# Performance work log

Measured on AMD Instinct MI355X. Metric: run time of the kernel, lower is better.

Reference implementation:

```python
import jax, jax.numpy as jnp
import numpy as np

P = 2        # patch size (all 3 dims)
NB = 8       # num_bands
N = 16       # d_state
DTR = 8      # dt_rank = d_model // 16
DCONV = 4    # d_conv
SMAX = 2.0   # smax_dt = smax_B = smax_C


def _ln(x, g, b):
    mu = x.mean(-1, keepdims=True)
    v = ((x - mu) ** 2).mean(-1, keepdims=True)
    return (x - mu) / jnp.sqrt(v + 1e-5) * g + b


def _silu(x):
    return x * jax.nn.sigmoid(x)


def _ssm_layer(x, band, m, rho, Win, bin_, convw, convb, Wx, Wdt, bdt, Alog, Dp,
               Wout, bout, edt, eB, eC, wr, wm):
    # x: [B, L, d_model] -> bidirectional conditioned selective scan (BiFCSSM)
    Bsz, L, _ = x.shape
    ED = convw.shape[0]
    xz = x @ Win + bin_
    xp, z = xz[..., :ED], xz[..., ED:]
    # depthwise causal conv1d over L
    xpad = jnp.pad(xp, ((0, 0), (DCONV - 1, 0), (0, 0)))
    xc = sum(xpad[:, k:k + L, :] * convw[:, k] for k in range(DCONV)) + convb
    xc = _silu(xc)
    dbl = xc @ Wx                                    # [B,L,DTR+2N]
    dt = jax.nn.softplus(dbl[..., :DTR] @ Wdt + bdt)  # [B,L,ED]
    # band/radius/mask conditioned modulation of delta, B, C
    s_dt = SMAX * jax.nn.sigmoid(edt[band][None] + wr[0] * rho[None] + wm[0] * m)
    s_B = SMAX * jax.nn.sigmoid(eB[band][None] + wr[1] * rho[None] + wm[1] * m)
    s_C = SMAX * jax.nn.sigmoid(eC[band][None] + wr[2] * rho[None] + wm[2] * m)
    dt = dt * s_dt[..., None]
    Bm = dbl[..., DTR:DTR + N] * s_B[..., None]       # [B,L,N]
    Cm = dbl[..., DTR + N:] * s_C[..., None]          # [B,L,N]
    A = -jnp.exp(Alog)                                # [ED,N]
    dA = jnp.exp(dt[..., None] * A)                   # [B,L,ED,N]
    dBu = (dA - 1.0) / A * Bm[:, :, None, :] * xc[..., None]   # exact ZOH
    dA_s = jnp.moveaxis(dA, 1, 0)
    dBu_s = jnp.moveaxis(dBu, 1, 0)
    C_s = jnp.moveaxis(Cm, 1, 0)
    h0 = jnp.zeros((Bsz, ED, N), x.dtype)

    def step(h, inp):
        a, bu, c = inp
        h = a * h + bu
        return h, jnp.einsum('ben,bn->be', h, c)

    _, yf = jax.lax.scan(step, h0, (dA_s, dBu_s, C_s))
    _, yb = jax.lax.scan(step, h0, (dA_s, dBu_s, C_s), reverse=True)
    y = jnp.moveaxis(yf + yb, 0, 1) + Dp * xc
    y = y * _silu(z)
    return y @ Wout + bout


def _fwd(kspace_ri, mask, pe_w, pe_b, pu_w, pu_b, ln_g, ln_b, fn_g, fn_b,
         cond_band, cond_rad_w, cond_mask_w, l0_Win, l0_bin, l0_convw, l0_convb,
         l0_Wx, l0_Wdt, l0_bdt, l0_Alog, l0_D, l0_Wout, l0_bout, l0_edt, l0_eB,
         l0_eC, l0_wr, l0_wm):
    Bsz, C, nx, ny, nz = kspace_ri.shape
    gx, gy, gz = nx // P, ny // P, nz // P
    L = gx * gy * gz
    # patch embed (Conv3d, kernel==stride) as blocked einsum
    xr = kspace_ri.reshape(Bsz, C, gx, P, gy, P, gz, P)
    x = jnp.einsum('bcxiyjzk,dcijk->bdxyz', xr, pe_w) + pe_b[None, :, None, None, None]
    DM = x.shape[1]
    x = x.reshape(Bsz, DM, L).transpose(0, 2, 1)               # [B,L,D]
    m = mask.reshape(Bsz, 1, gx, P, gy, P, gz, P).mean(axis=(3, 5, 7)).reshape(Bsz, L)
    m = jnp.clip(m, 0.0, 1.0)
    # raster scan ordering: identity permutation, rho_bar, band ids
    rho = jnp.arange(L, dtype=x.dtype) / float(L - 1)
    band = jnp.clip(jnp.floor(rho * NB).astype(jnp.int32), 0, NB - 1)
    # condition tokens
    cond = cond_band[band][None] + rho[None, :, None] * cond_rad_w + m[:, :, None] * cond_mask_w
    h = _ln(x + cond, ln_g, ln_b)
    h = h + _ssm_layer(_ln(h, fn_g, fn_b), band, m, rho, l0_Win, l0_bin, l0_convw,
                       l0_convb, l0_Wx, l0_Wdt, l0_bdt, l0_Alog, l0_D, l0_Wout,
                       l0_bout, l0_edt, l0_eB, l0_eC, l0_wr, l0_wm)
    # patch unembed (ConvTranspose3d, kernel==stride) as blocked einsum
    hg = h.transpose(0, 2, 1).reshape(Bsz, DM, gx, gy, gz)
    out = jnp.einsum('bdxyz,dcijk->bcxiyjzk', hg, pu_w).reshape(Bsz, C, nx, ny, nz)
    out = out + pu_b[None, :, None, None, None]
    return kspace_ri + out


def setup_inputs() -> dict:
    key = jax.random.key(0)
    ks = jax.random.split(key, 24)
    ED, DM, CIN = 256, 128, 16

    def nrm(k, shape, s):
        return jax.random.normal(k, shape, jnp.float32) * s

    return {
        'kspace_ri': jax.random.normal(ks[0], (1, CIN, 64, 64, 16), jnp.float32),
        'mask': jax.random.uniform(ks[1], (1, 1, 64, 64, 16), jnp.float32),
        'pe_w': nrm(ks[2], (DM, CIN, P, P, P), 0.09),
        'pe_b': nrm(ks[3], (DM,), 0.02),
        'pu_w': nrm(ks[4], (DM, CIN, P, P, P), 0.05),
        'pu_b': jnp.zeros((CIN,), jnp.float32),
        'ln_g': jnp.ones((DM,), jnp.float32),
        'ln_b': jnp.zeros((DM,), jnp.float32),
        'fn_g': jnp.ones((DM,), jnp.float32),
        'fn_b': jnp.zeros((DM,), jnp.float32),
        'cond_band': nrm(ks[5], (NB, DM), 0.02),
        'cond_rad_w': nrm(ks[6], (DM,), 0.02),
        'cond_mask_w': nrm(ks[7], (DM,), 0.02),
        'l0_Win': nrm(ks[8], (DM, 2 * ED), 0.05),
        'l0_bin': jnp.zeros((2 * ED,), jnp.float32),
        'l0_convw': nrm(ks[9], (ED, DCONV), 0.2),
        'l0_convb': jnp.zeros((ED,), jnp.float32),
        'l0_Wx': nrm(ks[10], (ED, DTR + 2 * N), 0.05),
        'l0_Wdt': nrm(ks[11], (DTR, ED), 0.1),
        'l0_bdt': jnp.full((ED,), -3.0, jnp.float32),
        'l0_Alog': jnp.log(jnp.tile(jnp.arange(1, N + 1, dtype=jnp.float32), (ED, 1))),
        'l0_D': jnp.ones((ED,), jnp.float32),
        'l0_Wout': nrm(ks[12], (ED, DM), 0.05),
        'l0_bout': jnp.zeros((DM,), jnp.float32),
        'l0_edt': nrm(ks[13], (NB,), 0.1),
        'l0_eB': nrm(ks[14], (NB,), 0.1),
        'l0_eC': nrm(ks[15], (NB,), 0.1),
        'l0_wr': nrm(ks[16], (3,), 0.1),
        'l0_wm': nrm(ks[17], (3,), 0.1),
    }


def reference(kspace_ri, mask, pe_w, pe_b, pu_w, pu_b, ln_g, ln_b, fn_g, fn_b,
              cond_band, cond_rad_w, cond_mask_w, l0_Win, l0_bin, l0_convw,
              l0_convb, l0_Wx, l0_Wdt, l0_bdt, l0_Alog, l0_D, l0_Wout, l0_bout,
              l0_edt, l0_eB, l0_eC, l0_wr, l0_wm):
    return _fwd(kspace_ri, mask, pe_w, pe_b, pu_w, pu_b, ln_g, ln_b, fn_g, fn_b,
                cond_band, cond_rad_w, cond_mask_w, l0_Win, l0_bin, l0_convw,
                l0_convb, l0_Wx, l0_Wdt, l0_bdt, l0_Alog, l0_D, l0_Wout, l0_bout,
                l0_edt, l0_eB, l0_eC, l0_wr, l0_wm)
```

## Files before the change

### kernel.cpp

```cpp
#include <hip/hip_runtime.h>
#include <hip/hip_bf16.h>

#define L_TOK 8192
#define NCh 256
#define CLh 32
#define LOG2E 1.44269504088896f

typedef short bf16x8 __attribute__((ext_vector_type(8)));
typedef float f32x4 __attribute__((ext_vector_type(4)));

static __device__ __forceinline__ float nexp2(float x) {
#if __has_builtin(__builtin_amdgcn_exp2f)
    return __builtin_amdgcn_exp2f(x);
#else
    return exp2f(x);
#endif
}
static __device__ __forceinline__ float sigm(float x) {
    return 1.f / (1.f + nexp2(-x * LOG2E));
}

static __device__ __forceinline__ ushort f2bf(float x) {
    union { float f; uint u; } v; v.f = x;
    uint r = v.u + 0x7fffu + ((v.u >> 16) & 1u);
// ... 62 lines not shown
        }
    }
    ushort h, lo; f2hl(v, &h, &lo);
    wH[i] = h; wL[i] = lo;
}

__global__ __launch_bounds__(256) void embed_ln_k(const float* __restrict__ ks,
                                                  const ushort* __restrict__ wH, const ushort* __restrict__ wL,
                                                  const float* __restrict__ pe_b, const float* __restrict__ cond_band,
                                                  const float* __restrict__ cond_rad, const float* __restrict__ cond_mask,
                                                  const float* __restrict__ mbuf,
                                                  const float* __restrict__ ln_g, const float* __restrict__ ln_b,
                                                  const float* __restrict__ fn_g, const float* __restrict__ fn_b,
                                                  float* __restrict__ h_,
                                                  ushort* __restrict__ hnH, ushort* __restrict__ hnL) {
    __shared__ __align__(16) char smem[46080];
    ushort (*AsH)[72] = (ushort(*)[72])(smem);
    ushort (*AsL)[72] = (ushort(*)[72])(smem + 4608);
    ushort (*BsH)[72] = (ushort(*)[72])(smem + 9216);
    ushort (*BsL)[72] = (ushort(*)[72])(smem + 27648);
    float  (*Cs)[132] = (float(*)[132])(smem);

    const int tid = threadIdx.x;
    const int lane = tid & 63, wn = tid >> 6;
    const int ln = lane & 15, q = lane >> 4;
    const int mb = blockIdx.x * 32;

    f32x4 acc[2][2];
#pragma unroll
    for (int rb = 0; rb < 2; ++rb)
#pragma unroll
        for (int cb = 0; cb < 2; ++cb) acc[rb][cb] = (f32x4){0.f, 0.f, 0.f, 0.f};

    for (int kc = 0; kc < 128; kc += 64) {
        __syncthreads();
        for (int u = tid; u < 2048; u += 256) {
            int r = u >> 6, kk = u & 63;
            int l = mb + r, k = kc + kk;
            int cc = k >> 3, ijk = k & 7;
            int xg = l >> 8, yg = (l >> 3) & 31, zg = l & 7;
            int i2 = (ijk >> 2) & 1, j2 = (ijk >> 1) & 1, k2 = ijk & 1;
            float v = ks[cc * 65536 + (2 * xg + i2) * 1024 + (2 * yg + j2) * 16 + 2 * zg + k2];
            ushort h, lo; f2hl(v, &h, &lo);
            AsH[r][kk] = h; AsL[r][kk] = lo;
        }
        for (int u = tid; u < 1024; u += 256) {
            int n = u >> 3, g = u & 7;
            *(uint4*)&BsH[n][g * 8] = *(const uint4*)&wH[W_PE + n * 128 + kc + g * 8];
            *(uint4*)&BsL[n][g * 8] = *(const uint4*)&wL[W_PE + n * 128 + kc + g * 8];
        }
        __syncthreads();
#pragma unroll
        for (int ks_ = 0; ks_ < 64; ks_ += 32) {
            const int kk = ks_ + q * 8;
            bf16x8 ah[2], al[2], bh[2], bl[2];
#pragma unroll
            for (int rb = 0; rb < 2; ++rb) {
                ah[rb] = *(const bf16x8*)&AsH[rb * 16 + ln][kk];
                al[rb] = *(const bf16x8*)&AsL[rb * 16 + ln][kk];
            }
#pragma unroll
            for (int cb = 0; cb < 2; ++cb) {
                bh[cb] = *(const bf16x8*)&BsH[wn * 32 + cb * 16 + ln][kk];
                bl[cb] = *(const bf16x8*)&BsL[wn * 32 + cb * 16 + ln][kk];
            }
#pragma unroll
            for (int rb = 0; rb < 2; ++rb)
#pragma unroll
                for (int cb = 0; cb < 2; ++cb) {
                    acc[rb][cb] = __builtin_amdgcn_mfma_f32_16x16x32_bf16(ah[rb], bh[cb], acc[rb][cb], 0, 0, 0);
                    acc[rb][cb] = __builtin_amdgcn_mfma_f32_16x16x32_bf16(ah[rb], bl[cb], acc[rb][cb], 0, 0, 0);
                    acc[rb][cb] = __builtin_amdgcn_mfma_f32_16x16x32_bf16(al[rb], bh[cb], acc[rb][cb], 0, 0, 0);
                }
        }
    }
    __syncthreads();
#pragma unroll
    for (int rb = 0; rb < 2; ++rb) {
#pragma unroll
        for (int cb = 0; cb < 2; ++cb) {
#pragma unroll
            for (int r = 0; r < 4; ++r) {
                int row = rb * 16 + q * 4 + r;
                int col = wn * 32 + cb * 16 + ln;
                int l = mb + row;
                float rho = (float)l * (1.0f / 8191.0f);
                int band = min(7, (int)(rho * 8.0f));
                Cs[row][col] = acc[rb][cb][r] + pe_b[col] + cond_band[band * 128 + col]
                               + rho * cond_rad[col] + mbuf[l] * cond_mask[col];
            }
        }
    }
    __syncthreads();
    {
        int row = tid >> 3, j = tid & 7;
        int l = mb + row;
        float v16[16];
        float s = 0.f, s2 = 0.f;
#pragma unroll
        for (int i = 0; i < 16; ++i) {
            float v = Cs[row][j * 16 + i];
            v16[i] = v; s += v; s2 += v * v;
        }
#pragma unroll
        for (int o = 1; o < 8; o <<= 1) { s += __shfl_xor(s, o, 8); s2 += __shfl_xor(s2, o, 8); }
        float mu = s * (1.f / 128.f);
        float var = s2 * (1.f / 128.f) - mu * mu;
        float rstd = rsqrtf(fmaxf(var, 0.f) + 1e-5f);
        float hv[16];
        s = 0.f; s2 = 0.f;
#pragma unroll
        for (int i = 0; i < 16; ++i) {
            int col = j * 16 + i;
            float h = (v16[i] - mu) * rstd * ln_g[col] + ln_b[col];
            hv[i] = h; s += h; s2 += h * h;
        }
#pragma unroll
        for (int i = 0; i < 16; i += 4)
            *(float4*)&h_[(size_t)l * 128 + j * 16 + i] = make_float4(hv[i], hv[i + 1], hv[i + 2], hv[i + 3]);
#pragma unroll
        for (int o = 1; o < 8; o <<= 1) { s += __shfl_xor(s, o, 8); s2 += __shfl_xor(s2, o, 8); }
        mu = s * (1.f / 128.f);
        var = s2 * (1.f / 128.f) - mu * mu;
        rstd = rsqrtf(fmaxf(var, 0.f) + 1e-5f);
        union { ushort u[16]; uint4 v4[2]; } oh, ol;
#pragma unroll
        for (int i = 0; i < 16; ++i) {
            int col = j * 16 + i;
            float o2 = (hv[i] - mu) * rstd * fn_g[col] + fn_b[col];
            ushort hh, ll; f2hl(o2, &hh, &ll);
            oh.u[i] = hh; ol.u[i] = ll;
        }
        *(uint4*)&hnH[(size_t)l * 128 + j * 16] = oh.v4[0];
        *(uint4*)&hnH[(size_t)l * 128 + j * 16 + 8] = oh.v4[1];
        *(uint4*)&hnL[(size_t)l * 128 + j * 16] = ol.v4[0];
        *(uint4*)&hnL[(size_t)l * 128 + j * 16 + 8] = ol.v4[1];
    }
}

__global__ __launch_bounds__(256) void win_k(const ushort* __restrict__ Ah, const ushort* __restrict__ Al,
                                             const ushort* __restrict__ wH, const ushort* __restrict__ wL,
                                             const float* __restrict__ bin_,
                                             float* __restrict__ xp, float* __restrict__ sz) {
    __shared__ ushort AsH[128][72], AsL[128][72];
    __shared__ ushort BsH[64][72], BsL[64][72];
    const int tid = threadIdx.x;
    const int lane = tid & 63, wave = tid >> 6;
    const int wm = wave & 1, wn = wave >> 1;
    const int ln = lane & 15, q = lane >> 4;
    const int mb = blockIdx.x * 128, nb = blockIdx.y * 64;

    f32x4 acc[4][2];
#pragma unroll
    for (int rb = 0; rb < 4; ++rb)
#pragma unroll
        for (int cb = 0; cb < 2; ++cb) acc[rb][cb] = (f32x4){0.f, 0.f, 0.f, 0.f};

    for (int kc = 0; kc < 128; kc += 64) {
        __syncthreads();
        for (int u = tid; u < 1024; u += 256) {
            int r = u >> 3, g = u & 7;
            size_t go = (size_t)(mb + r) * 128 + kc + g * 8;
            *(uint4*)&AsH[r][g * 8] = *(const uint4*)&Ah[go];
            *(uint4*)&AsL[r][g * 8] = *(const uint4*)&Al[go];
        }
        for (int u = tid; u < 512; u += 256) {
            int n = u >> 3, g = u & 7;
            size_t go = (size_t)(W_WIN) + (size_t)(nb + n) * 128 + kc + g * 8;
            *(uint4*)&BsH[n][g * 8] = *(const uint4*)&wH[go];
            *(uint4*)&BsL[n][g * 8] = *(const uint4*)&wL[go];
        }
        __syncthreads();
#pragma unroll
        for (int ks_ = 0; ks_ < 64; ks_ += 32) {
            const int kk = ks_ + q * 8;
            bf16x8 ah[4], al[4], bh[2], bl[2];
#pragma unroll
            for (int rb = 0; rb < 4; ++rb) {
                ah[rb] = *(const bf16x8*)&AsH[wm * 64 + rb * 16 + ln][kk];
                al[rb] = *(const bf16x8*)&AsL[wm * 64 + rb * 16 + ln][kk];
            }
#pragma unroll
            for (int cb = 0; cb < 2; ++cb) {
                bh[cb] = *(const bf16x8*)&BsH[wn * 32 + cb * 16 + ln][kk];
                bl[cb] = *(const bf16x8*)&BsL[wn * 32 + cb * 16 + ln][kk];
            }
#pragma unroll
            for (int rb = 0; rb < 4; ++rb)
#pragma unroll
                for (int cb = 0; cb < 2; ++cb) {
                    acc[rb][cb] = __builtin_amdgcn_mfma_f32_16x16x32_bf16(ah[rb], bh[cb], acc[rb][cb], 0, 0, 0);
                    acc[rb][cb] = __builtin_amdgcn_mfma_f32_16x16x32_bf16(ah[rb], bl[cb], acc[rb][cb], 0, 0, 0);
                    acc[rb][cb] = __builtin_amdgcn_mfma_f32_16x16x32_bf16(al[rb], bh[cb], acc[rb][cb], 0, 0, 0);
                }
        }
    }
#pragma unroll
    for (int rb = 0; rb < 4; ++rb)
#pragma unroll
        for (int cb = 0; cb < 2; ++cb)
#pragma unroll
            for (int r = 0; r < 4; ++r) {
                int l = mb + wm * 64 + rb * 16 + q * 4 + r;
                int col = nb + wn * 32 + cb * 16 + ln;
                float v = acc[rb][cb][r] + bin_[col];
                if (col < 256) {
                    xp[(size_t)l * 256 + col] = v;
                } else {
                    sz[(size_t)l * 256 + (col - 256)] = v * sigm(v);
                }
            }
}

__global__ __launch_bounds__(256) void conv_k(const float* __restrict__ xp, const float* __restrict__ convw,
                                              const float* __restrict__ convb, float* __restrict__ xc) {
    int id = blockIdx.x * 256 + threadIdx.x;
    int l = id >> 6, e4 = (id & 63) * 4;
    float4 cw[4];
// ... 15 lines not shown
    float4 r;
    r.x = o[0] * sigm(o[0]);
    r.y = o[1] * sigm(o[1]);
    r.z = o[2] * sigm(o[2]);
    r.w = o[3] * sigm(o[3]);
    *(float4*)&xc[(size_t)l * 256 + e4] = r;
}

__global__ __launch_bounds__(256) void proj_k(const float* __restrict__ xc,
                                              const ushort* __restrict__ wH, const ushort* __restrict__ wL,
                                              const float* __restrict__ bdt, const float* __restrict__ mbuf,
                                              const float* __restrict__ edt, const float* __restrict__ eB,
                                              const float* __restrict__ eC, const float* __restrict__ wr,
                                              const float* __restrict__ wm,
                                              float* __restrict__ dt, float* __restrict__ Bm, float* __restrict__ Cm) {
    __shared__ ushort AsH[128][72], AsL[128][72];
    __shared__ ushort BsH[64][72], BsL[64][72];
    const int tid = threadIdx.x;
    const int lane = tid & 63, wave = tid >> 6;
    const int wm_ = wave & 1, wn = wave >> 1;
    const int ln = lane & 15, q = lane >> 4;
    const int mb = blockIdx.x * 128, nb = blockIdx.y * 64;

    f32x4 acc[4][2];
#pragma unroll
    for (int rb = 0; rb < 4; ++rb)
#pragma unroll
        for (int cb = 0; cb < 2; ++cb) acc[rb][cb] = (f32x4){0.f, 0.f, 0.f, 0.f};

    for (int kc = 0; kc < 256; kc += 64) {
        __syncthreads();
        for (int u = tid; u < 2048; u += 256) {
            int r = u >> 4, kq = u & 15;
            float4 v = *(const float4*)&xc[(size_t)(mb + r) * 256 + kc + kq * 4];
            union { ushort u[4]; uint2 v2; } hh, ll;
            f2hl(v.x, &hh.u[0], &ll.u[0]); f2hl(v.y, &hh.u[1], &ll.u[1]);
            f2hl(v.z, &hh.u[2], &ll.u[2]); f2hl(v.w, &hh.u[3], &ll.u[3]);
            *(uint2*)&AsH[r][kq * 4] = hh.v2;
            *(uint2*)&AsL[r][kq * 4] = ll.v2;
        }
        for (int u = tid; u < 512; u += 256) {
            int n = u >> 3, g = u & 7;
            size_t go = (size_t)(W_PROJ) + (size_t)(nb + n) * 256 + kc + g * 8;
            *(uint4*)&BsH[n][g * 8] = *(const uint4*)&wH[go];
            *(uint4*)&BsL[n][g * 8] = *(const uint4*)&wL[go];
        }
        __syncthreads();
#pragma unroll
        for (int ks_ = 0; ks_ < 64; ks_ += 32) {
            const int kk = ks_ + q * 8;
            bf16x8 ah[4], al[4], bh[2], bl[2];
#pragma unroll
            for (int rb = 0; rb < 4; ++rb) {
                ah[rb] = *(const bf16x8*)&AsH[wm_ * 64 + rb * 16 + ln][kk];
                al[rb] = *(const bf16x8*)&AsL[wm_ * 64 + rb * 16 + ln][kk];
            }
#pragma unroll
            for (int cb = 0; cb < 2; ++cb) {
                bh[cb] = *(const bf16x8*)&BsH[wn * 32 + cb * 16 + ln][kk];
                bl[cb] = *(const bf16x8*)&BsL[wn * 32 + cb * 16 + ln][kk];
            }
#pragma unroll
            for (int rb = 0; rb < 4; ++rb)
#pragma unroll
                for (int cb = 0; cb < 2; ++cb) {
                    acc[rb][cb] = __builtin_amdgcn_mfma_f32_16x16x32_bf16(ah[rb], bh[cb], acc[rb][cb], 0, 0, 0);
                    acc[rb][cb] = __builtin_amdgcn_mfma_f32_16x16x32_bf16(ah[rb], bl[cb], acc[rb][cb], 0, 0, 0);
                    acc[rb][cb] = __builtin_amdgcn_mfma_f32_16x16x32_bf16(al[rb], bh[cb], acc[rb][cb], 0, 0, 0);
                }
        }
    }
#pragma unroll
    for (int rb = 0; rb < 4; ++rb)
#pragma unroll
        for (int cb = 0; cb < 2; ++cb)
#pragma unroll
            for (int r = 0; r < 4; ++r) {
                int l = mb + wm_ * 64 + rb * 16 + q * 4 + r;
                int col = nb + wn * 32 + cb * 16 + ln;
                float v = acc[rb][cb][r];
                float rho = (float)l * (1.0f / 8191.0f);
                int band = min(7, (int)(rho * 8.0f));
                float mv = mbuf[l];
                if (col < 256) {
                    float sc0 = 2.0f * sigm(edt[band] + wr[0] * rho + wm[0] * mv);
                    float v2 = v + bdt[col];
                    float sp = (v2 > 20.f) ? v2 : log1pf(expf(v2));
                    dt[(size_t)l * 256 + col] = sp * sc0;
                } else if (col < 272) {
                    float sc1 = 2.0f * sigm(eB[band] + wr[1] * rho + wm[1] * mv);
                    Bm[(size_t)l * 16 + (col - 256)] = v * sc1;
                } else if (col < 288) {
                    float sc2 = 2.0f * sigm(eC[band] + wr[2] * rho + wm[2] * mv);
// ... 80 lines not shown
            if (PHASE == 1) yp[(size_t)(base + p) * 256 + e] = y;
        }
#pragma unroll
        for (int j = 0; j < 8; ++j) { cu[j] = nu[j]; cx[j] = nx[j]; }
    }
    if (PHASE == 0) {
#pragma unroll
        for (int j = 0; j < 4; ++j) {
            float4 hv = make_float4(h[4 * j], h[4 * j + 1], h[4 * j + 2], h[4 * j + 3]);
            *(float4*)&Hb[hofs + 4 * j] = hv;
        }
        if (dir == 0) sdtb[c * 256 + e] = sdt;
    }
}

__global__ __launch_bounds__(256) void combine_k(float* __restrict__ Hb, const float* __restrict__ sdtb,
                                                 const float* __restrict__ Alog) {
    int id = blockIdx.x * 256 + threadIdx.x;
    int dir = id >> 12, en = id & 4095, e = en >> 4;
    float A2 = -nexp2(Alog[en] * LOG2E) * LOG2E;
    float hi = 0.f;
    for (int g = 0; g < NCh / 8; ++g) {
        float Pv[8], qv[8];
#pragma unroll
        for (int j = 0; j < 8; ++j) {
            int c = dir ? (NCh - 1 - (g * 8 + j)) : (g * 8 + j);
            Pv[j] = sdtb[c * 256 + e];
            qv[j] = Hb[(size_t)(dir * NCh + c) * 4096 + en];
        }
#pragma unroll
        for (int j = 0; j < 8; ++j) {
            int c = dir ? (NCh - 1 - (g * 8 + j)) : (g * 8 + j);
            float P = nexp2(A2 * Pv[j]);
            Hb[(size_t)(dir * NCh + c) * 4096 + en] = hi;
            hi = P * hi + qv[j];
        }
    }
}

__global__ __launch_bounds__(256) void wout_k(const float* __restrict__ yf, const float* __restrict__ yb,
                                              const float* __restrict__ xc, const float* __restrict__ sz,
                                              const float* __restrict__ Dp,
                                              const ushort* __restrict__ wH, const ushort* __restrict__ wL,
                                              const float* __restrict__ bout, const float* __restrict__ h_,
                                              ushort* __restrict__ hfH, ushort* __restrict__ hfL) {
    __shared__ ushort AsH[64][72], AsL[64][72];
    __shared__ ushort BsH[64][72], BsL[64][72];
    const int tid = threadIdx.x;
    const int lane = tid & 63, wave = tid >> 6;
    const int wm = wave & 1, wn = wave >> 1;
    const int ln = lane & 15, q = lane >> 4;
    const int mb = blockIdx.x * 64, nb = blockIdx.y * 64;

    f32x4 acc[2][2];
#pragma unroll
    for (int rb = 0; rb < 2; ++rb)
#pragma unroll
        for (int cb = 0; cb < 2; ++cb) acc[rb][cb] = (f32x4){0.f, 0.f, 0.f, 0.f};

    for (int kc = 0; kc < 256; kc += 64) {
        __syncthreads();
        for (int u = tid; u < 1024; u += 256) {
            int r = u >> 4, kq = u & 15;
            size_t go = (size_t)(mb + r) * 256 + kc + kq * 4;
            float4 a = *(const float4*)&yf[go];
            float4 b = *(const float4*)&yb[go];
            float4 x = *(const float4*)&xc[go];
            float4 s = *(const float4*)&sz[go];
            float4 d = *(const float4*)&Dp[kc + kq * 4];
            float v0 = (a.x + b.x + d.x * x.x) * s.x;
            float v1 = (a.y + b.y + d.y * x.y) * s.y;
            float v2 = (a.z + b.z + d.z * x.z) * s.z;
            float v3 = (a.w + b.w + d.w * x.w) * s.w;
            union { ushort u[4]; uint2 v2; } hh, ll;
            f2hl(v0, &hh.u[0], &ll.u[0]); f2hl(v1, &hh.u[1], &ll.u[1]);
            f2hl(v2, &hh.u[2], &ll.u[2]); f2hl(v3, &hh.u[3], &ll.u[3]);
            *(uint2*)&AsH[r][kq * 4] = hh.v2;
            *(uint2*)&AsL[r][kq * 4] = ll.v2;
        }
        for (int u = tid; u < 512; u += 256) {
            int n = u >> 3, g = u & 7;
            size_t go = (size_t)(W_WOUT) + (size_t)(nb + n) * 256 + kc + g * 8;
            *(uint4*)&BsH[n][g * 8] = *(const uint4*)&wH[go];
            *(uint4*)&BsL[n][g * 8] = *(const uint4*)&wL[go];
        }
        __syncthreads();
#pragma unroll
        for (int ks_ = 0; ks_ < 64; ks_ += 32) {
            const int kk = ks_ + q * 8;
            bf16x8 ah[2], al[2], bh[2], bl[2];
#pragma unroll
            for (int rb = 0; rb < 2; ++rb) {
                ah[rb] = *(const bf16x8*)&AsH[wm * 32 + rb * 16 + ln][kk];
                al[rb] = *(const bf16x8*)&AsL[wm * 32 + rb * 16 + ln][kk];
            }
#pragma unroll
            for (int cb = 0; cb < 2; ++cb) {
                bh[cb] = *(const bf16x8*)&BsH[wn * 32 + cb * 16 + ln][kk];
                bl[cb] = *(const bf16x8*)&BsL[wn * 32 + cb * 16 + ln][kk];
            }
#pragma unroll
            for (int rb = 0; rb < 2; ++rb)
#pragma unroll
                for (int cb = 0; cb < 2; ++cb) {
                    acc[rb][cb] = __builtin_amdgcn_mfma_f32_16x16x32_bf16(ah[rb], bh[cb], acc[rb][cb], 0, 0, 0);
                    acc[rb][cb] = __builtin_amdgcn_mfma_f32_16x16x32_bf16(ah[rb], bl[cb], acc[rb][cb], 0, 0, 0);
                    acc[rb][cb] = __builtin_amdgcn_mfma_f32_16x16x32_bf16(al[rb], bh[cb], acc[rb][cb], 0, 0, 0);
                }
        }
    }
#pragma unroll
    for (int rb = 0; rb < 2; ++rb)
#pragma unroll
        for (int cb = 0; cb < 2; ++cb)
#pragma unroll
            for (int r = 0; r < 4; ++r) {
                int l = mb + wm * 32 + rb * 16 + q * 4 + r;
                int col = nb + wn * 32 + cb * 16 + ln;
                float v = acc[rb][cb][r] + bout[col] + h_[(size_t)l * 128 + col];
                ushort hh, ll; f2hl(v, &hh, &ll);
                hfH[(size_t)l * 128 + col] = hh;
                hfL[(size_t)l * 128 + col] = ll;
            }
}

__global__ __launch_bounds__(256) void unembed_k(const ushort* __restrict__ Ah, const ushort* __restrict__ Al,
                                                 const ushort* __restrict__ wH, const ushort* __restrict__ wL,
                                                 const float* __restrict__ pu_b, const float* __restrict__ ks,
                                                 float* __restrict__ out) {
    __shared__ ushort AsH[64][72], AsL[64][72];
    __shared__ ushort BsH[64][72], BsL[64][72];
    const int tid = threadIdx.x;
    const int lane = tid & 63, wave = tid >> 6;
    const int wm = wave & 1, wn = wave >> 1;
    const int ln = lane & 15, q = lane >> 4;
    const int mb = blockIdx.x * 64, nb = blockIdx.y * 64;

    f32x4 acc[2][2];
#pragma unroll
    for (int rb = 0; rb < 2; ++rb)
#pragma unroll
        for (int cb = 0; cb < 2; ++cb) acc[rb][cb] = (f32x4){0.f, 0.f, 0.f, 0.f};

    for (int kc = 0; kc < 128; kc += 64) {
        __syncthreads();
        for (int u = tid; u < 512; u += 256) {
            int r = u >> 3, g = u & 7;
            size_t go = (size_t)(mb + r) * 128 + kc + g * 8;
            *(uint4*)&AsH[r][g * 8] = *(const uint4*)&Ah[go];
            *(uint4*)&AsL[r][g * 8] = *(const uint4*)&Al[go];
        }
        for (int u = tid; u < 512; u += 256) {
            int n = u >> 3, g = u & 7;
            size_t go = (size_t)(W_PU) + (size_t)(nb + n) * 128 + kc + g * 8;
            *(uint4*)&BsH[n][g * 8] = *(const uint4*)&wH[go];
            *(uint4*)&BsL[n][g * 8] = *(const uint4*)&wL[go];
        }
        __syncthreads();
#pragma unroll
        for (int ks_ = 0; ks_ < 64; ks_ += 32) {
            const int kk = ks_ + q * 8;
            bf16x8 ah[2], al[2], bh[2], bl[2];
#pragma unroll
            for (int rb = 0; rb < 2; ++rb) {
                ah[rb] = *(const bf16x8*)&AsH[wm * 32 + rb * 16 + ln][kk];
                al[rb] = *(const bf16x8*)&AsL[wm * 32 + rb * 16 + ln][kk];
            }
#pragma unroll
            for (int cb = 0; cb < 2; ++cb) {
                bh[cb] = *(const bf16x8*)&BsH[wn * 32 + cb * 16 + ln][kk];
                bl[cb] = *(const bf16x8*)&BsL[wn * 32 + cb * 16 + ln][kk];
            }
#pragma unroll
            for (int rb = 0; rb < 2; ++rb)
#pragma unroll
                for (int cb = 0; cb < 2; ++cb) {
                    acc[rb][cb] = __builtin_amdgcn_mfma_f32_16x16x32_bf16(ah[rb], bh[cb], acc[rb][cb], 0, 0, 0);
                    acc[rb][cb] = __builtin_amdgcn_mfma_f32_16x16x32_bf16(ah[rb], bl[cb], acc[rb][cb], 0, 0, 0);
                    acc[rb][cb] = __builtin_amdgcn_mfma_f32_16x16x32_bf16(al[rb], bh[cb], acc[rb][cb], 0, 0, 0);
                }
        }
    }
#pragma unroll
    for (int rb = 0; rb < 2; ++rb)
#pragma unroll
        for (int cb = 0; cb < 2; ++cb)
#pragma unroll
            for (int r = 0; r < 4; ++r) {
                int l = mb + wm * 32 + rb * 16 + q * 4 + r;
                int col = nb + wn * 32 + cb * 16 + ln;
                int xg = l >> 8, yg = (l >> 3) & 31, zg = l & 7;
                int c = col >> 3, ijk = col & 7;
                int i2 = (ijk >> 2) & 1, j2 = (ijk >> 1) & 1, k2 = ijk & 1;
                size_t idx = (size_t)((c * 64 + 2 * xg + i2) * 64 + (2 * yg + j2)) * 16 + 2 * zg + k2;
                out[idx] = acc[rb][cb][r] + pu_b[c] + ks[idx];
            }
}

extern "C" void kernel_launch(void* const* d_in, const int* in_sizes, int n_in,
                              void* d_out, int out_size, void* d_ws, size_t ws_size,
                              hipStream_t stream) {
    const float* ks    = (const float*)d_in[0];
    const float* mask  = (const float*)d_in[1];
    const float* pe_w  = (const float*)d_in[2];
    const float* pe_b  = (const float*)d_in[3];
    const float* pu_w  = (const float*)d_in[4];
    const float* pu_b  = (const float*)d_in[5];
    const float* ln_g  = (const float*)d_in[6];
    const float* ln_b  = (const float*)d_in[7];
    const float* fn_g  = (const float*)d_in[8];
    const float* fn_b  = (const float*)d_in[9];
// ... 22 lines not shown
    size_t o = 0;
    auto alloc = [&](size_t bytes) { char* p = base + o; o += (bytes + 255) & ~(size_t)255; return p; };
    float*  mbuf = (float*)alloc(32768);
    ushort* wH   = (ushort*)alloc(W_TOT * 2);
    ushort* wL   = (ushort*)alloc(W_TOT * 2);
    float*  h_   = (float*)alloc(4194304);
    ushort* hnH  = (ushort*)alloc(2097152);
    ushort* hnL  = (ushort*)alloc(2097152);
    float*  xp   = (float*)alloc(8388608);
    float*  sz   = (float*)alloc(8388608);
    float*  xc   = (float*)alloc(8388608);
    float*  dt   = (float*)alloc(8388608);
    float*  Bm   = (float*)alloc(524288);
    float*  Cm   = (float*)alloc(524288);
    float*  Hb   = (float*)alloc(8388608);
    float*  sdtb = (float*)alloc(262144);
    float*  yf   = (float*)alloc(8388608);
    float*  yb   = (float*)alloc(8388608);
    ushort* hfH  = (ushort*)alloc(2097152);
    ushort* hfL  = (ushort*)alloc(2097152);

    prep_k<<<864, 256, 0, stream>>>(pe_w, Win, Wx, Wdt, Wout, pu_w, mask, wH, wL, mbuf);
    embed_ln_k<<<256, 256, 0, stream>>>(ks, wH, wL, pe_b, cond_band, cond_rad, cond_mask, mbuf,
                                        ln_g, ln_b, fn_g, fn_b, h_, hnH, hnL);
    win_k<<<dim3(64, 8), 256, 0, stream>>>(hnH, hnL, wH, wL, bin_, xp, sz);
    conv_k<<<2048, 256, 0, stream>>>(xp, convw, convb, xc);
    proj_k<<<dim3(64, 5), 256, 0, stream>>>(xc, wH, wL, bdt, mbuf, edt, eB, eC, wr, wm, dt, Bm, Cm);
    scan_k<0><<<dim3(NCh, 2), 256, 0, stream>>>(dt, xc, Bm, Cm, Alog, Hb, sdtb, nullptr, nullptr);
    combine_k<<<32, 256, 0, stream>>>(Hb, sdtb, Alog);
    scan_k<1><<<dim3(NCh, 2), 256, 0, stream>>>(dt, xc, Bm, Cm, Alog, Hb, sdtb, yf, yb);
    wout_k<<<dim3(128, 2), 256, 0, stream>>>(yf, yb, xc, sz, Dp, wH, wL, bout, h_, hfH, hfL);
    unembed_k<<<dim3(128, 2), 256, 0, stream>>>(hfH, hfL, wH, wL, pu_b, ks, out);
}
```

Before: 258.8 us.

## Halve GEMM row tiles to double grid sizes and split combine output buffer

Halves the M-tile size in the embed, Win, proj, Wout and unembed GEMM kernels, doubling their block counts so more CUs are busy on this small token count. The combine kernel now uses 64-thread blocks across 128 blocks and writes prefix states to a separate Hpre buffer instead of overwriting Hb in place. This trades weight-tile reuse per block for more parallelism, and adds an extra 8 MB workspace buffer.

```diff
diff --git a/kernel.cpp b/kernel.cpp
--- a/kernel.cpp
+++ b/kernel.cpp
@@ -100,27 +100,25 @@
                                                   const float* __restrict__ fn_g, const float* __restrict__ fn_b,
                                                   float* __restrict__ h_,
                                                   ushort* __restrict__ hnH, ushort* __restrict__ hnL) {
-    __shared__ __align__(16) char smem[46080];
+    __shared__ __align__(16) char smem[41472];
     ushort (*AsH)[72] = (ushort(*)[72])(smem);
-    ushort (*AsL)[72] = (ushort(*)[72])(smem + 4608);
-    ushort (*BsH)[72] = (ushort(*)[72])(smem + 9216);
-    ushort (*BsL)[72] = (ushort(*)[72])(smem + 27648);
+    ushort (*AsL)[72] = (ushort(*)[72])(smem + 2304);
+    ushort (*BsH)[72] = (ushort(*)[72])(smem + 4608);
+    ushort (*BsL)[72] = (ushort(*)[72])(smem + 23040);
     float  (*Cs)[132] = (float(*)[132])(smem);
 
     const int tid = threadIdx.x;
     const int lane = tid & 63, wn = tid >> 6;
     const int ln = lane & 15, q = lane >> 4;
-    const int mb = blockIdx.x * 32;
-
-    f32x4 acc[2][2];
-#pragma unroll
-    for (int rb = 0; rb < 2; ++rb)
-#pragma unroll
-        for (int cb = 0; cb < 2; ++cb) acc[rb][cb] = (f32x4){0.f, 0.f, 0.f, 0.f};
+    const int mb = blockIdx.x * 16;
+
+    f32x4 acc[2];
+    acc[0] = (f32x4){0.f, 0.f, 0.f, 0.f};
+    acc[1] = (f32x4){0.f, 0.f, 0.f, 0.f};
 
     for (int kc = 0; kc < 128; kc += 64) {
         __syncthreads();
-        for (int u = tid; u < 2048; u += 256) {
+        for (int u = tid; u < 1024; u += 256) {
             int r = u >> 6, kk = u & 63;
             int l = mb + r, k = kc + kk;
             int cc = k >> 3, ijk = k & 7;
@@ -139,11 +137,118 @@
 #pragma unroll
         for (int ks_ = 0; ks_ < 64; ks_ += 32) {
             const int kk = ks_ + q * 8;
+            bf16x8 ah = *(const bf16x8*)&AsH[ln][kk];
+            bf16x8 al = *(const bf16x8*)&AsL[ln][kk];
+#pragma unroll
+            for (int cb = 0; cb < 2; ++cb) {
+                bf16x8 bh = *(const bf16x8*)&BsH[wn * 32 + cb * 16 + ln][kk];
+                bf16x8 bl = *(const bf16x8*)&BsL[wn * 32 + cb * 16 + ln][kk];
+                acc[cb] = __builtin_amdgcn_mfma_f32_16x16x32_bf16(ah, bh, acc[cb], 0, 0, 0);
+                acc[cb] = __builtin_amdgcn_mfma_f32_16x16x32_bf16(ah, bl, acc[cb], 0, 0, 0);
+                acc[cb] = __builtin_amdgcn_mfma_f32_16x16x32_bf16(al, bh, acc[cb], 0, 0, 0);
+            }
+        }
+    }
+    __syncthreads();
+#pragma unroll
+    for (int cb = 0; cb < 2; ++cb) {
+#pragma unroll
+        for (int r = 0; r < 4; ++r) {
+            int row = q * 4 + r;
+            int col = wn * 32 + cb * 16 + ln;
+            int l = mb + row;
+            float rho = (float)l * (1.0f / 8191.0f);
+            int band = min(7, (int)(rho * 8.0f));
+            Cs[row][col] = acc[cb][r] + pe_b[col] + cond_band[band * 128 + col]
+                           + rho * cond_rad[col] + mbuf[l] * cond_mask[col];
+        }
+    }
+    __syncthreads();
+    {
+        int row = tid >> 4, j = tid & 15;
+        int l = mb + row;
+        float v8[8];
+        float s = 0.f, s2 = 0.f;
+#pragma unroll
+        for (int i = 0; i < 8; ++i) {
+            float v = Cs[row][j * 8 + i];
+            v8[i] = v; s += v; s2 += v * v;
+        }
+#pragma unroll
+        for (int o = 1; o < 16; o <<= 1) { s += __shfl_xor(s, o, 16); s2 += __shfl_xor(s2, o, 16); }
+        float mu = s * (1.f / 128.f);
+        float var = s2 * (1.f / 128.f) - mu * mu;
+        float rstd = rsqrtf(fmaxf(var, 0.f) + 1e-5f);
+        float hv[8];
+        s = 0.f; s2 = 0.f;
+#pragma unroll
+        for (int i = 0; i < 8; ++i) {
+            int col = j * 8 + i;
+            float h = (v8[i] - mu) * rstd * ln_g[col] + ln_b[col];
+            hv[i] = h; s += h; s2 += h * h;
+        }
+#pragma unroll
+        for (int i = 0; i < 8; i += 4)
+            *(float4*)&h_[(size_t)l * 128 + j * 8 + i] = make_float4(hv[i], hv[i + 1], hv[i + 2], hv[i + 3]);
+#pragma unroll
+        for (int o = 1; o < 16; o <<= 1) { s += __shfl_xor(s, o, 16); s2 += __shfl_xor(s2, o, 16); }
+        mu = s * (1.f / 128.f);
+        var = s2 * (1.f / 128.f) - mu * mu;
+        rstd = rsqrtf(fmaxf(var, 0.f) + 1e-5f);
+        union { ushort u[8]; uint4 v4; } oh, ol;
+#pragma unroll
+        for (int i = 0; i < 8; ++i) {
+            int col = j * 8 + i;
+            float o2 = (hv[i] - mu) * rstd * fn_g[col] + fn_b[col];
+            ushort hh, ll; f2hl(o2, &hh, &ll);
+            oh.u[i] = hh; ol.u[i] = ll;
+        }
+        *(uint4*)&hnH[(size_t)l * 128 + j * 8] = oh.v4;
+        *(uint4*)&hnL[(size_t)l * 128 + j * 8] = ol.v4;
+    }
+}
+
+__global__ __launch_bounds__(256) void win_k(const ushort* __restrict__ Ah, const ushort* __restrict__ Al,
+                                             const ushort* __restrict__ wH, const ushort* __restrict__ wL,
+                                             const float* __restrict__ bin_,
+                                             float* __restrict__ xp, float* __restrict__ sz) {
+    __shared__ ushort AsH[64][72], AsL[64][72];
+    __shared__ ushort BsH[64][72], BsL[64][72];
+    const int tid = threadIdx.x;
+    const int lane = tid & 63, wave = tid >> 6;
+    const int wm = wave & 1, wn = wave >> 1;
+    const int ln = lane & 15, q = lane >> 4;
+    const int mb = blockIdx.x * 64, nb = blockIdx.y * 64;
+
+    f32x4 acc[2][2];
+#pragma unroll
+    for (int rb = 0; rb < 2; ++rb)
+#pragma unroll
+        for (int cb = 0; cb < 2; ++cb) acc[rb][cb] = (f32x4){0.f, 0.f, 0.f, 0.f};
+
+    for (int kc = 0; kc < 128; kc += 64) {
+        __syncthreads();
+        for (int u = tid; u < 512; u += 256) {
+            int r = u >> 3, g = u & 7;
+            size_t go = (size_t)(mb + r) * 128 + kc + g * 8;
+            *(uint4*)&AsH[r][g * 8] = *(const uint4*)&Ah[go];
+            *(uint4*)&AsL[r][g * 8] = *(const uint4*)&Al[go];
+        }
+        for (int u = tid; u < 512; u += 256) {
+            int n = u >> 3, g = u & 7;
+            size_t go = (size_t)(W_WIN) + (size_t)(nb + n) * 128 + kc + g * 8;
+            *(uint4*)&BsH[n][g * 8] = *(const uint4*)&wH[go];
+            *(uint4*)&BsL[n][g * 8] = *(const uint4*)&wL[go];
+        }
+        __syncthreads();
+#pragma unroll
+        for (int ks_ = 0; ks_ < 64; ks_ += 32) {
+            const int kk = ks_ + q * 8;
             bf16x8 ah[2], al[2], bh[2], bl[2];
 #pragma unroll
             for (int rb = 0; rb < 2; ++rb) {
-                ah[rb] = *(const bf16x8*)&AsH[rb * 16 + ln][kk];
-                al[rb] = *(const bf16x8*)&AsL[rb * 16 + ln][kk];
+                ah[rb] = *(const bf16x8*)&AsH[wm * 32 + rb * 16 + ln][kk];
+                al[rb] = *(const bf16x8*)&AsL[wm * 32 + rb * 16 + ln][kk];
             }
 #pragma unroll
             for (int cb = 0; cb < 2; ++cb) {
@@ -160,134 +265,13 @@
                 }
         }
     }
-    __syncthreads();
-#pragma unroll
-    for (int rb = 0; rb < 2; ++rb) {
-#pragma unroll
-        for (int cb = 0; cb < 2; ++cb) {
+#pragma unroll
+    for (int rb = 0; rb < 2; ++rb)
+#pragma unroll
+        for (int cb = 0; cb < 2; ++cb)
 #pragma unroll
             for (int r = 0; r < 4; ++r) {
-                int row = rb * 16 + q * 4 + r;
-                int col = wn * 32 + cb * 16 + ln;
-                int l = mb + row;
-                float rho = (float)l * (1.0f / 8191.0f);
-                int band = min(7, (int)(rho * 8.0f));
-                Cs[row][col] = acc[rb][cb][r] + pe_b[col] + cond_band[band * 128 + col]
-                               + rho * cond_rad[col] + mbuf[l] * cond_mask[col];
-            }
-        }
-    }
-    __syncthreads();
-    {
-        int row = tid >> 3, j = tid & 7;
-        int l = mb + row;
-        float v16[16];
-        float s = 0.f, s2 = 0.f;
-#pragma unroll
-        for (int i = 0; i < 16; ++i) {
-            float v = Cs[row][j * 16 + i];
-            v16[i] = v; s += v; s2 += v * v;
-        }
-#pragma unroll
-        for (int o = 1; o < 8; o <<= 1) { s += __shfl_xor(s, o, 8); s2 += __shfl_xor(s2, o, 8); }
-        float mu = s * (1.f / 128.f);
-        float var = s2 * (1.f / 128.f) - mu * mu;
-        float rstd = rsqrtf(fmaxf(var, 0.f) + 1e-5f);
-        float hv[16];
-        s = 0.f; s2 = 0.f;
-#pragma unroll
-        for (int i = 0; i < 16; ++i) {
-            int col = j * 16 + i;
-            float h = (v16[i] - mu) * rstd * ln_g[col] + ln_b[col];
-            hv[i] = h; s += h; s2 += h * h;
-        }
-#pragma unroll
-        for (int i = 0; i < 16; i += 4)
-            *(float4*)&h_[(size_t)l * 128 + j * 16 + i] = make_float4(hv[i], hv[i + 1], hv[i + 2], hv[i + 3]);
-#pragma unroll
-        for (int o = 1; o < 8; o <<= 1) { s += __shfl_xor(s, o, 8); s2 += __shfl_xor(s2, o, 8); }
-        mu = s * (1.f / 128.f);
-        var = s2 * (1.f / 128.f) - mu * mu;
-        rstd = rsqrtf(fmaxf(var, 0.f) + 1e-5f);
-        union { ushort u[16]; uint4 v4[2]; } oh, ol;
-#pragma unroll
-        for (int i = 0; i < 16; ++i) {
-            int col = j * 16 + i;
-            float o2 = (hv[i] - mu) * rstd * fn_g[col] + fn_b[col];
-            ushort hh, ll; f2hl(o2, &hh, &ll);
-            oh.u[i] = hh; ol.u[i] = ll;
-        }
-        *(uint4*)&hnH[(size_t)l * 128 + j * 16] = oh.v4[0];
-        *(uint4*)&hnH[(size_t)l * 128 + j * 16 + 8] = oh.v4[1];
-        *(uint4*)&hnL[(size_t)l * 128 + j * 16] = ol.v4[0];
-        *(uint4*)&hnL[(size_t)l * 128 + j * 16 + 8] = ol.v4[1];
-    }
-}
-
-__global__ __launch_bounds__(256) void win_k(const ushort* __restrict__ Ah, const ushort* __restrict__ Al,
-                                             const ushort* __restrict__ wH, const ushort* __restrict__ wL,
-                                             const float* __restrict__ bin_,
-                                             float* __restrict__ xp, float* __restrict__ sz) {
-    __shared__ ushort AsH[128][72], AsL[128][72];
-    __shared__ ushort BsH[64][72], BsL[64][72];
-    const int tid = threadIdx.x;
-    const int lane = tid & 63, wave = tid >> 6;
-    const int wm = wave & 1, wn = wave >> 1;
-    const int ln = lane & 15, q = lane >> 4;
-    const int mb = blockIdx.x * 128, nb = blockIdx.y * 64;
-
-    f32x4 acc[4][2];
-#pragma unroll
-    for (int rb = 0; rb < 4; ++rb)
-#pragma unroll
-        for (int cb = 0; cb < 2; ++cb) acc[rb][cb] = (f32x4){0.f, 0.f, 0.f, 0.f};
-
-    for (int kc = 0; kc < 128; kc += 64) {
-        __syncthreads();
-        for (int u = tid; u < 1024; u += 256) {
-            int r = u >> 3, g = u & 7;
-            size_t go = (size_t)(mb + r) * 128 + kc + g * 8;
-            *(uint4*)&AsH[r][g * 8] = *(const uint4*)&Ah[go];
-            *(uint4*)&AsL[r][g * 8] = *(const uint4*)&Al[go];
-        }
-        for (int u = tid; u < 512; u += 256) {
-            int n = u >> 3, g = u & 7;
-            size_t go = (size_t)(W_WIN) + (size_t)(nb + n) * 128 + kc + g * 8;
-            *(uint4*)&BsH[n][g * 8] = *(const uint4*)&wH[go];
-            *(uint4*)&BsL[n][g * 8] = *(const uint4*)&wL[go];
-        }
-        __syncthreads();
-#pragma unroll
-        for (int ks_ = 0; ks_ < 64; ks_ += 32) {
-            const int kk = ks_ + q * 8;
-            bf16x8 ah[4], al[4], bh[2], bl[2];
-#pragma unroll
-            for (int rb = 0; rb < 4; ++rb) {
-                ah[rb] = *(const bf16x8*)&AsH[wm * 64 + rb * 16 + ln][kk];
-                al[rb] = *(const bf16x8*)&AsL[wm * 64 + rb * 16 + ln][kk];
-            }
-#pragma unroll
-            for (int cb = 0; cb < 2; ++cb) {
-                bh[cb] = *(const bf16x8*)&BsH[wn * 32 + cb * 16 + ln][kk];
-                bl[cb] = *(const bf16x8*)&BsL[wn * 32 + cb * 16 + ln][kk];
-            }
-#pragma unroll
-            for (int rb = 0; rb < 4; ++rb)
-#pragma unroll
-                for (int cb = 0; cb < 2; ++cb) {
-                    acc[rb][cb] = __builtin_amdgcn_mfma_f32_16x16x32_bf16(ah[rb], bh[cb], acc[rb][cb], 0, 0, 0);
-                    acc[rb][cb] = __builtin_amdgcn_mfma_f32_16x16x32_bf16(ah[rb], bl[cb], acc[rb][cb], 0, 0, 0);
-                    acc[rb][cb] = __builtin_amdgcn_mfma_f32_16x16x32_bf16(al[rb], bh[cb], acc[rb][cb], 0, 0, 0);
-                }
-        }
-    }
-#pragma unroll
-    for (int rb = 0; rb < 4; ++rb)
-#pragma unroll
-        for (int cb = 0; cb < 2; ++cb)
-#pragma unroll
-            for (int r = 0; r < 4; ++r) {
-                int l = mb + wm * 64 + rb * 16 + q * 4 + r;
+                int l = mb + wm * 32 + rb * 16 + q * 4 + r;
                 int col = nb + wn * 32 + cb * 16 + ln;
                 float v = acc[rb][cb][r] + bin_[col];
                 if (col < 256) {
@@ -333,23 +317,23 @@
                                               const float* __restrict__ eC, const float* __restrict__ wr,
                                               const float* __restrict__ wm,
                                               float* __restrict__ dt, float* __restrict__ Bm, float* __restrict__ Cm) {
-    __shared__ ushort AsH[128][72], AsL[128][72];
+    __shared__ ushort AsH[64][72], AsL[64][72];
     __shared__ ushort BsH[64][72], BsL[64][72];
     const int tid = threadIdx.x;
     const int lane = tid & 63, wave = tid >> 6;
     const int wm_ = wave & 1, wn = wave >> 1;
     const int ln = lane & 15, q = lane >> 4;
-    const int mb = blockIdx.x * 128, nb = blockIdx.y * 64;
-
-    f32x4 acc[4][2];
-#pragma unroll
-    for (int rb = 0; rb < 4; ++rb)
+    const int mb = blockIdx.x * 64, nb = blockIdx.y * 64;
+
+    f32x4 acc[2][2];
+#pragma unroll
+    for (int rb = 0; rb < 2; ++rb)
 #pragma unroll
         for (int cb = 0; cb < 2; ++cb) acc[rb][cb] = (f32x4){0.f, 0.f, 0.f, 0.f};
 
     for (int kc = 0; kc < 256; kc += 64) {
         __syncthreads();
-        for (int u = tid; u < 2048; u += 256) {
+        for (int u = tid; u < 1024; u += 256) {
             int r = u >> 4, kq = u & 15;
             float4 v = *(const float4*)&xc[(size_t)(mb + r) * 256 + kc + kq * 4];
             union { ushort u[4]; uint2 v2; } hh, ll;
@@ -368,11 +352,11 @@
 #pragma unroll
         for (int ks_ = 0; ks_ < 64; ks_ += 32) {
             const int kk = ks_ + q * 8;
-            bf16x8 ah[4], al[4], bh[2], bl[2];
-#pragma unroll
-            for (int rb = 0; rb < 4; ++rb) {
-                ah[rb] = *(const bf16x8*)&AsH[wm_ * 64 + rb * 16 + ln][kk];
-                al[rb] = *(const bf16x8*)&AsL[wm_ * 64 + rb * 16 + ln][kk];
+            bf16x8 ah[2], al[2], bh[2], bl[2];
+#pragma unroll
+            for (int rb = 0; rb < 2; ++rb) {
+                ah[rb] = *(const bf16x8*)&AsH[wm_ * 32 + rb * 16 + ln][kk];
+                al[rb] = *(const bf16x8*)&AsL[wm_ * 32 + rb * 16 + ln][kk];
             }
 #pragma unroll
             for (int cb = 0; cb < 2; ++cb) {
@@ -380,7 +364,7 @@
                 bl[cb] = *(const bf16x8*)&BsL[wn * 32 + cb * 16 + ln][kk];
             }
 #pragma unroll
-            for (int rb = 0; rb < 4; ++rb)
+            for (int rb = 0; rb < 2; ++rb)
 #pragma unroll
                 for (int cb = 0; cb < 2; ++cb) {
                     acc[rb][cb] = __builtin_amdgcn_mfma_f32_16x16x32_bf16(ah[rb], bh[cb], acc[rb][cb], 0, 0, 0);
@@ -390,12 +374,12 @@
         }
     }
 #pragma unroll
-    for (int rb = 0; rb < 4; ++rb)
+    for (int rb = 0; rb < 2; ++rb)
 #pragma unroll
         for (int cb = 0; cb < 2; ++cb)
 #pragma unroll
             for (int r = 0; r < 4; ++r) {
-                int l = mb + wm_ * 64 + rb * 16 + q * 4 + r;
+                int l = mb + wm_ * 32 + rb * 16 + q * 4 + r;
                 int col = nb + wn * 32 + cb * 16 + ln;
                 float v = acc[rb][cb][r];
                 float rho = (float)l * (1.0f / 8191.0f);
@@ -506,9 +490,9 @@
     }
 }
 
-__global__ __launch_bounds__(256) void combine_k(float* __restrict__ Hb, const float* __restrict__ sdtb,
-                                                 const float* __restrict__ Alog) {
-    int id = blockIdx.x * 256 + threadIdx.x;
+__global__ __launch_bounds__(64) void combine_k(const float* __restrict__ Hb, float* __restrict__ Hpre,
+                                                const float* __restrict__ sdtb, const float* __restrict__ Alog) {
+    int id = blockIdx.x * 64 + threadIdx.x;
     int dir = id >> 12, en = id & 4095, e = en >> 4;
     float A2 = -nexp2(Alog[en] * LOG2E) * LOG2E;
     float hi = 0.f;
@@ -524,7 +508,7 @@
         for (int j = 0; j < 8; ++j) {
             int c = dir ? (NCh - 1 - (g * 8 + j)) : (g * 8 + j);
             float P = nexp2(A2 * Pv[j]);
-            Hb[(size_t)(dir * NCh + c) * 4096 + en] = hi;
+            Hpre[(size_t)(dir * NCh + c) * 4096 + en] = hi;
             hi = P * hi + qv[j];
         }
     }
@@ -536,23 +520,21 @@
                                               const ushort* __restrict__ wH, const ushort* __restrict__ wL,
                                               const float* __restrict__ bout, const float* __restrict__ h_,
                                               ushort* __restrict__ hfH, ushort* __restrict__ hfL) {
-    __shared__ ushort AsH[64][72], AsL[64][72];
+    __shared__ ushort AsH[32][72], AsL[32][72];
     __shared__ ushort BsH[64][72], BsL[64][72];
     const int tid = threadIdx.x;
     const int lane = tid & 63, wave = tid >> 6;
     const int wm = wave & 1, wn = wave >> 1;
     const int ln = lane & 15, q = lane >> 4;
-    const int mb = blockIdx.x * 64, nb = blockIdx.y * 64;
-
-    f32x4 acc[2][2];
-#pragma unroll
-    for (int rb = 0; rb < 2; ++rb)
-#pragma unroll
-        for (int cb = 0; cb < 2; ++cb) acc[rb][cb] = (f32x4){0.f, 0.f, 0.f, 0.f};
+    const int mb = blockIdx.x * 32, nb = blockIdx.y * 64;
+
+    f32x4 acc[2];
+    acc[0] = (f32x4){0.f, 0.f, 0.f, 0.f};
+    acc[1] = (f32x4){0.f, 0.f, 0.f, 0.f};
 
     for (int kc = 0; kc < 256; kc += 64) {
         __syncthreads();
-        for (int u = tid; u < 1024; u += 256) {
+        for (int u = tid; u < 512; u += 256) {
             int r = u >> 4, kq = u & 15;
             size_t go = (size_t)(mb + r) * 256 + kc + kq * 4;
             float4 a = *(const float4*)&yf[go];
@@ -580,63 +562,50 @@
 #pragma unroll
         for (int ks_ = 0; ks_ < 64; ks_ += 32) {
             const int kk = ks_ + q * 8;
-            bf16x8 ah[2], al[2], bh[2], bl[2];
-#pragma unroll
-            for (int rb = 0; rb < 2; ++rb) {
-                ah[rb] = *(const bf16x8*)&AsH[wm * 32 + rb * 16 + ln][kk];
-                al[rb] = *(const bf16x8*)&AsL[wm * 32 + rb * 16 + ln][kk];
-            }
+            bf16x8 ah = *(const bf16x8*)&AsH[wm * 16 + ln][kk];
+            bf16x8 al = *(const bf16x8*)&AsL[wm * 16 + ln][kk];
 #pragma unroll
             for (int cb = 0; cb < 2; ++cb) {
-                bh[cb] = *(const bf16x8*)&BsH[wn * 32 + cb * 16 + ln][kk];
-                bl[cb] = *(const bf16x8*)&BsL[wn * 32 + cb * 16 + ln][kk];
-            }
-#pragma unroll
-            for (int rb = 0; rb < 2; ++rb)
-#pragma unroll
-                for (int cb = 0; cb < 2; ++cb) {
-                    acc[rb][cb] = __builtin_amdgcn_mfma_f32_16x16x32_bf16(ah[rb], bh[cb], acc[rb][cb], 0, 0, 0);
-                    acc[rb][cb] = __builtin_amdgcn_mfma_f32_16x16x32_bf16(ah[rb], bl[cb], acc[rb][cb], 0, 0, 0);
-                    acc[rb][cb] = __builtin_amdgcn_mfma_f32_16x16x32_bf16(al[rb], bh[cb], acc[rb][cb], 0, 0, 0);
-                }
-        }
-    }
-#pragma unroll
-    for (int rb = 0; rb < 2; ++rb)
-#pragma unroll
-        for (int cb = 0; cb < 2; ++cb)
-#pragma unroll
-            for (int r = 0; r < 4; ++r) {
-                int l = mb + wm * 32 + rb * 16 + q * 4 + r;
-                int col = nb + wn * 32 + cb * 16 + ln;
-                float v = acc[rb][cb][r] + bout[col] + h_[(size_t)l * 128 + col];
-                ushort hh, ll; f2hl(v, &hh, &ll);
-                hfH[(size_t)l * 128 + col] = hh;
-                hfL[(size_t)l * 128 + col] = ll;
-            }
+                bf16x8 bh = *(const bf16x8*)&BsH[wn * 32 + cb * 16 + ln][kk];
+                bf16x8 bl = *(const bf16x8*)&BsL[wn * 32 + cb * 16 + ln][kk];
+                acc[cb] = __builtin_amdgcn_mfma_f32_16x16x32_bf16(ah, bh, acc[cb], 0, 0, 0);
+                acc[cb] = __builtin_amdgcn_mfma_f32_16x16x32_bf16(ah, bl, acc[cb], 0, 0, 0);
+                acc[cb] = __builtin_amdgcn_mfma_f32_16x16x32_bf16(al, bh, acc[cb], 0, 0, 0);
+            }
+        }
+    }
+#pragma unroll
+    for (int cb = 0; cb < 2; ++cb)
+#pragma unroll
+        for (int r = 0; r < 4; ++r) {
+            int l = mb + wm * 16 + q * 4 + r;
+            int col = nb + wn * 32 + cb * 16 + ln;
+            float v = acc[cb][r] + bout[col] + h_[(size_t)l * 128 + col];
+            ushort hh, ll; f2hl(v, &hh, &ll);
+            hfH[(size_t)l * 128 + col] = hh;
+            hfL[(size_t)l * 128 + col] = ll;
+        }
 }
 
 __global__ __launch_bounds__(256) void unembed_k(const ushort* __restrict__ Ah, const ushort* __restrict__ Al,
                                                  const ushort* __restrict__ wH, const ushort* __restrict__ wL,
                                                  const float* __restrict__ pu_b, const float* __restrict__ ks,
                                                  float* __restrict__ out) {
-    __shared__ ushort AsH[64][72], AsL[64][72];
+    __shared__ ushort AsH[32][72], AsL[32][72];
     __shared__ ushort BsH[64][72], BsL[64][72];
     const int tid = threadIdx.x;
     const int lane = tid & 63, wave = tid >> 6;
     const int wm = wave & 1, wn = wave >> 1;
     const int ln = lane & 15, q = lane >> 4;
-    const int mb = blockIdx.x * 64, nb = blockIdx.y * 64;
-
-    f32x4 acc[2][2];
-#pragma unroll
-    for (int rb = 0; rb < 2; ++rb)
-#pragma unroll
-        for (int cb = 0; cb < 2; ++cb) acc[rb][cb] = (f32x4){0.f, 0.f, 0.f, 0.f};
+    const int mb = blockIdx.x * 32, nb = blockIdx.y * 64;
+
+    f32x4 acc[2];
+    acc[0] = (f32x4){0.f, 0.f, 0.f, 0.f};
+    acc[1] = (f32x4){0.f, 0.f, 0.f, 0.f};
 
     for (int kc = 0; kc < 128; kc += 64) {
         __syncthreads();
-        for (int u = tid; u < 512; u += 256) {
+        for (int u = tid; u < 256; u += 256) {
             int r = u >> 3, g = u & 7;
             size_t go = (size_t)(mb + r) * 128 + kc + g * 8;
             *(uint4*)&AsH[r][g * 8] = *(const uint4*)&Ah[go];
@@ -652,41 +621,30 @@
 #pragma unroll
         for (int ks_ = 0; ks_ < 64; ks_ += 32) {
             const int kk = ks_ + q * 8;
-            bf16x8 ah[2], al[2], bh[2], bl[2];
-#pragma unroll
-            for (int rb = 0; rb < 2; ++rb) {
-                ah[rb] = *(const bf16x8*)&AsH[wm * 32 + rb * 16 + ln][kk];
-                al[rb] = *(const bf16x8*)&AsL[wm * 32 + rb * 16 + ln][kk];
-            }
+            bf16x8 ah = *(const bf16x8*)&AsH[wm * 16 + ln][kk];
+            bf16x8 al = *(const bf16x8*)&AsL[wm * 16 + ln][kk];
 #pragma unroll
             for (int cb = 0; cb < 2; ++cb) {
-                bh[cb] = *(const bf16x8*)&BsH[wn * 32 + cb * 16 + ln][kk];
-                bl[cb] = *(const bf16x8*)&BsL[wn * 32 + cb * 16 + ln][kk];
-            }
-#pragma unroll
-            for (int rb = 0; rb < 2; ++rb)
-#pragma unroll
-                for (int cb = 0; cb < 2; ++cb) {
-                    acc[rb][cb] = __builtin_amdgcn_mfma_f32_16x16x32_bf16(ah[rb], bh[cb], acc[rb][cb], 0, 0, 0);
-                    acc[rb][cb] = __builtin_amdgcn_mfma_f32_16x16x32_bf16(ah[rb], bl[cb], acc[rb][cb], 0, 0, 0);
-                    acc[rb][cb] = __builtin_amdgcn_mfma_f32_16x16x32_bf16(al[rb], bh[cb], acc[rb][cb], 0, 0, 0);
-                }
-        }
-    }
-#pragma unroll
-    for (int rb = 0; rb < 2; ++rb)
-#pragma unroll
-        for (int cb = 0; cb < 2; ++cb)
-#pragma unroll
-            for (int r = 0; r < 4; ++r) {
-                int l = mb + wm * 32 + rb * 16 + q * 4 + r;
-                int col = nb + wn * 32 + cb * 16 + ln;
-                int xg = l >> 8, yg = (l >> 3) & 31, zg = l & 7;
-                int c = col >> 3, ijk = col & 7;
-                int i2 = (ijk >> 2) & 1, j2 = (ijk >> 1) & 1, k2 = ijk & 1;
-                size_t idx = (size_t)((c * 64 + 2 * xg + i2) * 64 + (2 * yg + j2)) * 16 + 2 * zg + k2;
-                out[idx] = acc[rb][cb][r] + pu_b[c] + ks[idx];
-            }
+                bf16x8 bh = *(const bf16x8*)&BsH[wn * 32 + cb * 16 + ln][kk];
+                bf16x8 bl = *(const bf16x8*)&BsL[wn * 32 + cb * 16 + ln][kk];
+                acc[cb] = __builtin_amdgcn_mfma_f32_16x16x32_bf16(ah, bh, acc[cb], 0, 0, 0);
+                acc[cb] = __builtin_amdgcn_mfma_f32_16x16x32_bf16(ah, bl, acc[cb], 0, 0, 0);
+                acc[cb] = __builtin_amdgcn_mfma_f32_16x16x32_bf16(al, bh, acc[cb], 0, 0, 0);
+            }
+        }
+    }
+#pragma unroll
+    for (int cb = 0; cb < 2; ++cb)
+#pragma unroll
+        for (int r = 0; r < 4; ++r) {
+            int l = mb + wm * 16 + q * 4 + r;
+            int col = nb + wn * 32 + cb * 16 + ln;
+            int xg = l >> 8, yg = (l >> 3) & 31, zg = l & 7;
+            int c = col >> 3, ijk = col & 7;
+            int i2 = (ijk >> 2) & 1, j2 = (ijk >> 1) & 1, k2 = ijk & 1;
+            size_t idx = (size_t)((c * 64 + 2 * xg + i2) * 64 + (2 * yg + j2)) * 16 + 2 * zg + k2;
+            out[idx] = acc[cb][r] + pu_b[c] + ks[idx];
+        }
 }
 
 extern "C" void kernel_launch(void* const* d_in, const int* in_sizes, int n_in,
@@ -739,6 +697,7 @@
     float*  Bm   = (float*)alloc(524288);
     float*  Cm   = (float*)alloc(524288);
     float*  Hb   = (float*)alloc(8388608);
+    float*  Hpre = (float*)alloc(8388608);
     float*  sdtb = (float*)alloc(262144);
     float*  yf   = (float*)alloc(8388608);
     float*  yb   = (float*)alloc(8388608);
@@ -746,14 +705,14 @@
     ushort* hfL  = (ushort*)alloc(2097152);
 
     prep_k<<<864, 256, 0, stream>>>(pe_w, Win, Wx, Wdt, Wout, pu_w, mask, wH, wL, mbuf);
-    embed_ln_k<<<256, 256, 0, stream>>>(ks, wH, wL, pe_b, cond_band, cond_rad, cond_mask, mbuf,
+    embed_ln_k<<<512, 256, 0, stream>>>(ks, wH, wL, pe_b, cond_band, cond_rad, cond_mask, mbuf,
                                         ln_g, ln_b, fn_g, fn_b, h_, hnH, hnL);
-    win_k<<<dim3(64, 8), 256, 0, stream>>>(hnH, hnL, wH, wL, bin_, xp, sz);
+    win_k<<<dim3(128, 8), 256, 0, stream>>>(hnH, hnL, wH, wL, bin_, xp, sz);
     conv_k<<<2048, 256, 0, stream>>>(xp, convw, convb, xc);
-    proj_k<<<dim3(64, 5), 256, 0, stream>>>(xc, wH, wL, bdt, mbuf, edt, eB, eC, wr, wm, dt, Bm, Cm);
+    proj_k<<<dim3(128, 5), 256, 0, stream>>>(xc, wH, wL, bdt, mbuf, edt, eB, eC, wr, wm, dt, Bm, Cm);
     scan_k<0><<<dim3(NCh, 2), 256, 0, stream>>>(dt, xc, Bm, Cm, Alog, Hb, sdtb, nullptr, nullptr);
-    combine_k<<<32, 256, 0, stream>>>(Hb, sdtb, Alog);
-    scan_k<1><<<dim3(NCh, 2), 256, 0, stream>>>(dt, xc, Bm, Cm, Alog, Hb, sdtb, yf, yb);
-    wout_k<<<dim3(128, 2), 256, 0, stream>>>(yf, yb, xc, sz, Dp, wH, wL, bout, h_, hfH, hfL);
-    unembed_k<<<dim3(128, 2), 256, 0, stream>>>(hfH, hfL, wH, wL, pu_b, ks, out);
-}
+    combine_k<<<128, 64, 0, stream>>>(Hb, Hpre, sdtb, Alog);
+    scan_k<1><<<dim3(NCh, 2), 256, 0, stream>>>(dt, xc, Bm, Cm, Alog, Hpre, sdtb, yf, yb);
+    wout_k<<<dim3(256, 2), 256, 0, stream>>>(yf, yb, xc, sz, Dp, wH, wL, bout, h_, hfH, hfL);
+    unembed_k<<<dim3(256, 2), 256, 0, stream>>>(hfH, hfL, wH, wL, pu_b, ks, out);
+}
```

Result: faster. 239.9 us (-7.3%).
